# Kernel tuning notes

Measured on AMD Instinct MI355X. Metric: run time of the kernel, lower is better.

The kernel has to match this reference:

```python
import jax, jax.numpy as jnp
import numpy as np

N, D, L, K = 32, 128, 3136, 64

def setup_inputs() -> dict:
    key = jax.random.key(0)
    k1, k2, k3 = jax.random.split(key, 3)
    x = jax.random.normal(k1, (N, D, L), dtype=jnp.float32)
    weight = jax.random.normal(k2, (K, D), dtype=jnp.float32)  # codebook centers
    scale = jax.random.normal(k3, (1,), dtype=jnp.float32)
    return {"x": x, "weight": weight, "scale": scale}

def reference(x, weight, scale):
    # x: (N, C, ...) -> (N, D, L); output scaled squared L2 dist (N, K, L)
    n, c = x.shape[0], x.shape[1]
    xf = x.reshape(n, c, -1)  # (N, D, L)
    x_sq = jnp.sum(xf * xf, axis=1)          # (N, L)
    c_sq = jnp.sum(weight * weight, axis=1)  # (K,)
    xc = jnp.einsum('ndl,kd->nkl', xf, weight)  # (N, K, L)
    dist = x_sq[:, None, :] + c_sq[None, :, None] - 2.0 * xc
    return dist / (scale[0] ** 2)
```

## Files before the change

### kernel.cpp

```cpp
#include <hip/hip_runtime.h>

#define N_ 32
#define D_ 128
#define L_ 3136
#define K_ 64

typedef _Float16 f16x8 __attribute__((ext_vector_type(8)));
typedef float    f32x4 __attribute__((ext_vector_type(4)));

__global__ __launch_bounds__(64) void prep_kernel(
    const float* __restrict__ w,
    unsigned short* __restrict__ wh,
    float* __restrict__ csq)
{
    const int b = blockIdx.x, lane = threadIdx.x;
    if (b < 16) {
        const int dc = b >> 2, kt = b & 3;
        const int row = kt * 16 + (lane & 15);
        const int d0  = dc * 32 + (lane >> 4) * 8;
        const float* src = w + row * D_ + d0;
        __attribute__((aligned(16))) unsigned short h[8];
#pragma unroll
        for (int j = 0; j < 8; ++j) {
            _Float16 v = (_Float16)src[j];
            h[j] = *(const unsigned short*)&v;
        }
        const size_t off = (size_t)(b * 64 + lane) * 8;
        *(ushort4*)(wh + off)     = *(const ushort4*)(h);
        *(ushort4*)(wh + off + 4) = *(const ushort4*)(h + 4);
    } else {
        const float* wr = w + lane * D_;
        float s = 0.f;
#pragma unroll
        for (int d = 0; d < D_; d += 4) {
            float4 v = *(const float4*)(wr + d);
            s = fmaf(v.x, v.x, s); s = fmaf(v.y, v.y, s);
            s = fmaf(v.z, v.z, s); s = fmaf(v.w, v.w, s);
        }
        csq[lane] = s;
    }
}

__global__ __launch_bounds__(256, 6) void enc_mfma_kernel(
    const float* __restrict__ x,
    const unsigned short* __restrict__ wh,
    const float* __restrict__ csqg,
    const float* __restrict__ scale,
    float* __restrict__ out)
{
    __shared__ __attribute__((aligned(16))) unsigned short lds_w[8192];
    __shared__ float lds_csq[K_];

    const int t    = threadIdx.x;
    const int wave = t >> 6;
    const int lane = t & 63;
    const int col  = lane & 15;
    const int quad = lane >> 4;
    const int n    = blockIdx.y;
    const int l0   = blockIdx.x * 64;

    const float* xa = x + (size_t)n * D_ * L_ + l0 + wave * 16 + col;
    float xv[4][8];
#pragma unroll
    for (int dc = 0; dc < 4; ++dc) {
        const float* xp = xa + (size_t)(dc * 32 + quad * 8) * L_;
#pragma unroll
        for (int j = 0; j < 8; ++j) xv[dc][j] = xp[(size_t)j * L_];
    }

#pragma unroll
    for (int i = 0; i < 4; ++i) {
        const int c = wave * 4 + i;
        __builtin_amdgcn_global_load_lds(
            (const __attribute__((address_space(1))) unsigned int*)(wh + (size_t)c * 512 + lane * 8),
            (__attribute__((address_space(3))) unsigned int*)&lds_w[c * 512],
            16, 0, 0);
    }
    if (wave == 0) {
        __builtin_amdgcn_global_load_lds(
            (const __attribute__((address_space(1))) unsigned int*)(csqg + lane),
            (__attribute__((address_space(3))) unsigned int*)lds_csq,
            4, 0, 0);
    }
    __syncthreads();

    f32x4 acc[4];
#pragma unroll
    for (int kt = 0; kt < 4; ++kt) acc[kt] = (f32x4){0.f, 0.f, 0.f, 0.f};
    float xsq = 0.f;

#pragma unroll
    for (int dc = 0; dc < 4; ++dc) {
        union { f16x8 v; _Float16 e[8]; } af;
#pragma unroll
        for (int j = 0; j < 8; ++j) {
            const float v = xv[dc][j];
            xsq = fmaf(v, v, xsq);
            af.e[j] = (_Float16)v;
        }
#pragma unroll
        for (int kt = 0; kt < 4; ++kt) {
            const int fo = ((dc * 4 + kt) * 64 + lane) * 8;
            f16x8 bf = *(const f16x8*)&lds_w[fo];
            acc[kt] = __builtin_amdgcn_mfma_f32_16x16x32_f16(af.v, bf, acc[kt], 0, 0, 0);
        }
    }

    xsq += __shfl_xor(xsq, 16, 64);
    xsq += __shfl_xor(xsq, 32, 64);
    float xs[4];
#pragma unroll
    for (int r = 0; r < 4; ++r)
        xs[r] = __shfl(xsq, quad * 4 + r, 64);

    const float sc = scale[0];
    const float inv_s2 = 1.0f / (sc * sc);
    float* op = out + (size_t)n * K_ * L_ + l0 + wave * 16 + quad * 4;
#pragma unroll
    for (int kt = 0; kt < 4; ++kt) {
        const float cs = lds_csq[kt * 16 + col];
        float4 v;
        v.x = (xs[0] + cs - 2.0f * acc[kt][0]) * inv_s2;
        v.y = (xs[1] + cs - 2.0f * acc[kt][1]) * inv_s2;
        v.z = (xs[2] + cs - 2.0f * acc[kt][2]) * inv_s2;
        v.w = (xs[3] + cs - 2.0f * acc[kt][3]) * inv_s2;
        *(float4*)(op + (size_t)(kt * 16 + col) * L_) = v;
    }
}

extern "C" void kernel_launch(void* const* d_in, const int* in_sizes, int n_in,
                              void* d_out, int out_size, void* d_ws, size_t ws_size,
                              hipStream_t stream) {
    const float* x     = (const float*)d_in[0];
    const float* w     = (const float*)d_in[1];
    const float* scale = (const float*)d_in[2];
    float* out = (float*)d_out;

    unsigned short* wh  = (unsigned short*)d_ws;
    float*          csq = (float*)((char*)d_ws + 16384);

    prep_kernel<<<17, 64, 0, stream>>>(w, wh, csq);
    dim3 grid(L_ / 64, N_);
    enc_mfma_kernel<<<grid, 256, 0, stream>>>(x, wh, csq, scale, out);
}
```

Baseline: 98.99 us.

## Process four 64-column tiles per block to amortize codebook LDS staging

```diff
diff --git a/kernel.cpp b/kernel.cpp
--- a/kernel.cpp
+++ b/kernel.cpp
@@ -41,7 +41,79 @@
     }
 }
 
-__global__ __launch_bounds__(256, 6) void enc_mfma_kernel(
+template<int NS>
+__device__ __forceinline__ void compute_store(
+    const float* __restrict__ xa,
+    const unsigned short* __restrict__ lds_w,
+    const float* __restrict__ lds_csq,
+    float inv_s2,
+    float* __restrict__ opb,
+    int lane, int col, int quad)
+{
+    f32x4 acc[NS][4];
+#pragma unroll
+    for (int s = 0; s < NS; ++s)
+#pragma unroll
+        for (int kt = 0; kt < 4; ++kt) acc[s][kt] = (f32x4){0.f, 0.f, 0.f, 0.f};
+    float xsq[NS];
+#pragma unroll
+    for (int s = 0; s < NS; ++s) xsq[s] = 0.f;
+
+#pragma unroll
+    for (int dc = 0; dc < 4; ++dc) {
+        const float* xp = xa + (size_t)(dc * 32 + quad * 8) * L_;
+        float xv[NS][8];
+#pragma unroll
+        for (int j = 0; j < 8; ++j)
+#pragma unroll
+            for (int s = 0; s < NS; ++s)
+                xv[s][j] = xp[(size_t)j * L_ + s * 64];
+
+        union { f16x8 v; _Float16 e[8]; } af[NS];
+#pragma unroll
+        for (int s = 0; s < NS; ++s)
+#pragma unroll
+            for (int j = 0; j < 8; ++j) {
+                const float v = xv[s][j];
+                xsq[s] = fmaf(v, v, xsq[s]);
+                af[s].e[j] = (_Float16)v;
+            }
+
+#pragma unroll
+        for (int kt = 0; kt < 4; ++kt) {
+            f16x8 bf = *(const f16x8*)&lds_w[((dc * 4 + kt) * 64 + lane) * 8];
+#pragma unroll
+            for (int s = 0; s < NS; ++s)
+                acc[s][kt] = __builtin_amdgcn_mfma_f32_16x16x32_f16(af[s].v, bf, acc[s][kt], 0, 0, 0);
+        }
+    }
+
+    float xs[NS][4];
+#pragma unroll
+    for (int s = 0; s < NS; ++s) {
+        float v = xsq[s];
+        v += __shfl_xor(v, 16, 64);
+        v += __shfl_xor(v, 32, 64);
+#pragma unroll
+        for (int r = 0; r < 4; ++r)
+            xs[s][r] = __shfl(v, quad * 4 + r, 64);
+    }
+
+#pragma unroll
+    for (int s = 0; s < NS; ++s)
+#pragma unroll
+        for (int kt = 0; kt < 4; ++kt) {
+            const float cs = lds_csq[kt * 16 + col];
+            float4 v;
+            v.x = (xs[s][0] + cs - 2.0f * acc[s][kt][0]) * inv_s2;
+            v.y = (xs[s][1] + cs - 2.0f * acc[s][kt][1]) * inv_s2;
+            v.z = (xs[s][2] + cs - 2.0f * acc[s][kt][2]) * inv_s2;
+            v.w = (xs[s][3] + cs - 2.0f * acc[s][kt][3]) * inv_s2;
+            *(float4*)(opb + (size_t)(kt * 16 + col) * L_ + s * 64) = v;
+        }
+}
+
+__global__ __launch_bounds__(256, 3) void enc_mfma_kernel(
     const float* __restrict__ x,
     const unsigned short* __restrict__ wh,
     const float* __restrict__ csqg,
@@ -57,16 +129,7 @@
     const int col  = lane & 15;
     const int quad = lane >> 4;
     const int n    = blockIdx.y;
-    const int l0   = blockIdx.x * 64;
-
-    const float* xa = x + (size_t)n * D_ * L_ + l0 + wave * 16 + col;
-    float xv[4][8];
-#pragma unroll
-    for (int dc = 0; dc < 4; ++dc) {
-        const float* xp = xa + (size_t)(dc * 32 + quad * 8) * L_;
-#pragma unroll
-        for (int j = 0; j < 8; ++j) xv[dc][j] = xp[(size_t)j * L_];
-    }
+    const int l0   = blockIdx.x * 256;
 
 #pragma unroll
     for (int i = 0; i < 4; ++i) {
@@ -84,48 +147,15 @@
     }
     __syncthreads();
 
-    f32x4 acc[4];
-#pragma unroll
-    for (int kt = 0; kt < 4; ++kt) acc[kt] = (f32x4){0.f, 0.f, 0.f, 0.f};
-    float xsq = 0.f;
-
-#pragma unroll
-    for (int dc = 0; dc < 4; ++dc) {
-        union { f16x8 v; _Float16 e[8]; } af;
-#pragma unroll
-        for (int j = 0; j < 8; ++j) {
-            const float v = xv[dc][j];
-            xsq = fmaf(v, v, xsq);
-            af.e[j] = (_Float16)v;
-        }
-#pragma unroll
-        for (int kt = 0; kt < 4; ++kt) {
-            const int fo = ((dc * 4 + kt) * 64 + lane) * 8;
-            f16x8 bf = *(const f16x8*)&lds_w[fo];
-            acc[kt] = __builtin_amdgcn_mfma_f32_16x16x32_f16(af.v, bf, acc[kt], 0, 0, 0);
-        }
-    }
-
-    xsq += __shfl_xor(xsq, 16, 64);
-    xsq += __shfl_xor(xsq, 32, 64);
-    float xs[4];
-#pragma unroll
-    for (int r = 0; r < 4; ++r)
-        xs[r] = __shfl(xsq, quad * 4 + r, 64);
-
     const float sc = scale[0];
     const float inv_s2 = 1.0f / (sc * sc);
-    float* op = out + (size_t)n * K_ * L_ + l0 + wave * 16 + quad * 4;
-#pragma unroll
-    for (int kt = 0; kt < 4; ++kt) {
-        const float cs = lds_csq[kt * 16 + col];
-        float4 v;
-        v.x = (xs[0] + cs - 2.0f * acc[kt][0]) * inv_s2;
-        v.y = (xs[1] + cs - 2.0f * acc[kt][1]) * inv_s2;
-        v.z = (xs[2] + cs - 2.0f * acc[kt][2]) * inv_s2;
-        v.w = (xs[3] + cs - 2.0f * acc[kt][3]) * inv_s2;
-        *(float4*)(op + (size_t)(kt * 16 + col) * L_) = v;
-    }
+    const float* xa  = x   + (size_t)n * D_ * L_ + l0 + wave * 16 + col;
+    float*       opb = out + (size_t)n * K_ * L_ + l0 + wave * 16 + quad * 4;
+
+    if (l0 + 256 <= L_)
+        compute_store<4>(xa, lds_w, lds_csq, inv_s2, opb, lane, col, quad);
+    else
+        compute_store<1>(xa, lds_w, lds_csq, inv_s2, opb, lane, col, quad);
 }
 
 extern "C" void kernel_launch(void* const* d_in, const int* in_sizes, int n_in,
@@ -140,6 +170,6 @@
     float*          csq = (float*)((char*)d_ws + 16384);
 
     prep_kernel<<<17, 64, 0, stream>>>(w, wh, csq);
-    dim3 grid(L_ / 64, N_);
+    dim3 grid((L_ + 255) / 256, N_);
     enc_mfma_kernel<<<grid, 256, 0, stream>>>(x, wh, csq, scale, out);
 }
```

Result: slower. 101.3 us (+2.3%).
